# Kernel tuning notes

Measured on AMD Instinct MI355X. Metric: run time of the kernel, lower is better.

Reference implementation:

```python
import jax, jax.numpy as jnp
import numpy as np

C = 10  # cluster gap window; repo-level global constant in the original code


def _per_neuron(v, label):
    """Faithful vectorized translation of the per-(batch,neuron) Python loops.

    v:     [T] membrane potential trace
    label: scalar int target cluster count
    Returns (loss_contribution, num_cluster).
    """
    T = v.shape[0]
    t = jnp.arange(T, dtype=jnp.int32)
    spk = v >= 0.0                                   # spike positions (v >= 0)
    # exclusive prefix counts of spikes: csp[i] = #spikes in v[:i]
    csp = jnp.concatenate([jnp.zeros(1, jnp.int32), jnp.cumsum(spk.astype(jnp.int32))])
    lo = jnp.clip(t - C, 0, T)
    # a spike starts a new cluster iff no spike in the preceding C steps
    cnt_prev = csp[t] - csp[lo]
    is_start = spk & (cnt_prev == 0)
    num_cluster = jnp.sum(is_start.astype(jnp.int32))
    vmax = jnp.max(v)

    # ---- excess branch (label > num_cluster) ----
    # mask[t] = 1 iff some spike lies in [t-C, t+C]  (union of [first-C, last+C] per cluster)
    hi = jnp.clip(t + C + 1, 0, T)
    mask = (csp[hi] - csp[lo]) > 0
    full0 = jnp.all(mask)
    NEG = jnp.asarray(-1e30, v.dtype)
    m0 = jnp.max(jnp.where(mask, NEG, v))            # max over unmasked times (iter 0)
    tm = jnp.argmax(v)                               # original uses global argmax of v
    win = (t >= tm - C // 2) & (t <= tm + C // 2)
    mask2 = mask | win                               # mask after first loop iteration (fixed thereafter)
    full2 = jnp.all(mask2)
    # if mask2 full, remaining iterations pick a spike value (random in original; spikes have v>=0,
    # we use the deterministic surrogate vmax which is always a spike value when spikes exist)
    m_rest = jnp.where(full2, vmax, jnp.max(jnp.where(mask2, NEG, v)))
    label_f = label.astype(v.dtype)
    ncf = num_cluster.astype(v.dtype)
    dE = jnp.maximum(label_f - ncf, 1.0)             # safe denominator (branch-gated below)
    mean_excess = (m0 + (dE - 1.0) * m_rest) / dE
    excess_loss = jnp.where(full0, vmax, -mean_excess)

    # ---- deficit branch (label < num_cluster) ----
    BIG = T + 2 * C + 2
    lt = jax.lax.cummax(jnp.where(spk, t, -BIG))                 # nearest spike <= t
    rt = jax.lax.cummin(jnp.where(spk, t, BIG)[::-1])[::-1]      # nearest spike >= t
    in_span = (rt - lt) <= C                                     # t inside [first,last] of a cluster
    cid = jnp.cumsum(is_start.astype(jnp.int32)) - 1             # cluster id at time t
    K = T // (C + 1) + 1                                         # max possible clusters
    seg = jnp.where(in_span, cid, K)
    rec = jax.ops.segment_max(v, seg, num_segments=K + 1)[:K]    # per-cluster span max
    POS = jnp.asarray(1e30, v.dtype)
    rec = jnp.where(jnp.arange(K) < num_cluster, rec, POS)
    rec = jnp.sort(rec)                                          # ascending, real clusters first
    dD = jnp.maximum(ncf - label_f, 1.0)
    deficit_loss = jnp.sum(jnp.where(jnp.arange(K) < (num_cluster - label), rec, 0.0)) / dD

    contrib = jnp.where(label > num_cluster, excess_loss,
                        jnp.where(label < num_cluster, deficit_loss, 0.0))
    return contrib, num_cluster


def setup_inputs() -> dict:
    key = jax.random.key(0)
    k1, k2, k3 = jax.random.split(key, 3)
    B, T, N = 256, 500, 128
    vmem = jax.random.normal(k1, (B, T, N), dtype=jnp.float32)
    vlastmem = jax.random.normal(k2, (B, T, N), dtype=jnp.float32)
    labels_t = jax.random.randint(k3, (B, N), 0, 5, dtype=jnp.int32)
    return {"vmem": vmem, "vlastmem": vlastmem, "labels_t": labels_t, "ratio": 1}


def reference(vmem, vlastmem, labels_t, ratio):
    # vlastmem and ratio are unused in the original forward; kept for signature fidelity.
    vv = jnp.transpose(vmem, (0, 2, 1))  # [B, N, T]
    contrib, nclus = jax.vmap(jax.vmap(_per_neuron))(vv, labels_t)
    loss = jnp.sum(contrib)
    spike_output = nclus.astype(jnp.float32)  # [B, N] cluster counts
    return loss, spike_output
```

## Files before the change

kernel.cpp:

```cpp
#include <hip/hip_runtime.h>

namespace {
constexpr int CC    = 10;
constexpr int TT    = 500;
constexpr int NN    = 128;
constexpr int G     = 10;
constexpr int LSEG  = TT / G;
constexpr int HALO  = CC;
constexpr int NSLOT = 10;
constexpr int MAXG  = TT / (CC + 1) + 1;
}

__global__ __launch_bounds__(128, 5)
void seg_scan_kernel(const float* __restrict__ vmem, float* __restrict__ ws) {
    const int s   = blockIdx.x;
    const int b   = blockIdx.y;
    const int tid = threadIdx.x;
    const int a   = s * LSEG;
    const float* __restrict__ col = vmem + (size_t)b * TT * NN + tid;

    __shared__ float stg[5 * NN];

    float b0[10], b1[10], b2[10], b3[10] = {};
    auto load = [&](float (&d)[10], int c) {
        #pragma unroll
        for (int j = 0; j < 10; ++j) {
            int t = a + (-HALO + 10 * c + j);
            t = t < 0 ? 0 : (t > TT - 1 ? TT - 1 : t);
            d[j] = col[(size_t)t * NN];
        }
    };

    int   ls = -(1 << 20), lcount = 0, hdne = 0, tmn = 0, hasu = 0;
    float ccm = -1e30f, rmax = -1e30f, hdm = -1e30f, vmx = -1e30f, m0 = -1e30f;
    const bool firstSeg = (s == 0), lastSeg = (s == G - 1);
    #pragma unroll
    for (int i = 0; i < 5; ++i) stg[i * NN + tid] = 0.0f;

    auto scan = [&](const float (&cur)[10], const float (&prev)[10], int c) {
        #pragma unroll
        for (int j = 0; j < 10; ++j) {
            const int ofs = -HALO + 10 * c + j;
            const int t   = a + ofs;
            float v = cur[j];
            if ((ofs < 0 && firstSeg) || (ofs >= LSEG && lastSeg)) v = -1.0f;
            const bool spike = v >= 0.0f;
            if (ofs >= 0 && ofs < LSEG) {
                const float rm2 = fmaxf(rmax, v);
                if (spike) {
                    if (t - ls > CC) {
                        if (lcount > 0) stg[(lcount - 1) * NN + tid] = ccm;
                        ccm = v; ++lcount;
                    } else if (lcount == 0) { hdne = 1; hdm = fmaxf(hdm, rm2); }
                    else ccm = fmaxf(ccm, rm2);
                    rmax = -1e30f;
                } else rmax = rm2;
                if (v > vmx) { vmx = v; tmn = t; }
            }
            if (spike) ls = t;
            if (ofs >= HALO) {
                const float vu = prev[j];
                if (ls < t - 2 * CC) { hasu = 1; if (vu > m0) m0 = vu; }
            }
        }
    };

    load(b0, 0); load(b1, 1);
    load(b2, 2); scan(b0, b3, 0);
    load(b3, 3); scan(b1, b0, 1);
    load(b0, 4); scan(b2, b1, 2);
    load(b1, 5); scan(b3, b2, 3);
    load(b2, 6); scan(b0, b3, 4);
    scan(b1, b0, 5);
    scan(b2, b1, 6);

    if (lcount > 0) stg[(lcount - 1) * NN + tid] = ccm;

    float* __restrict__ wsl = ws + (size_t)(b * G + s) * NSLOT * NN + tid;
    #pragma unroll
    for (int i = 0; i < 5; ++i) wsl[i * NN] = stg[i * NN + tid];
    const int packed = lcount | (hdne << 3) | (hasu << 4) | (tmn << 5);
    wsl[5 * NN] = __int_as_float(packed);
    wsl[6 * NN] = hdm;
    wsl[7 * NN] = rmax;
    wsl[8 * NN] = vmx;
    wsl[9 * NN] = m0;
}

__global__ __launch_bounds__(64)
void merge_kernel(const float* __restrict__ vmem, const float* __restrict__ ws,
                  const int* __restrict__ labels, float* __restrict__ out) {
    const int bb = blockIdx.x, lane = threadIdx.x;
    const int b = bb >> 1, n = ((bb & 1) << 6) | lane;
    __shared__ float gl[MAXG * 64];
    __shared__ float wb[512];

    const float* __restrict__ wsb = ws + (size_t)b * G * NSLOT * NN + n;
    float f[2][10];
    auto loadSeg = [&](int slot, int s2) {
        const float* p = wsb + (size_t)s2 * NSLOT * NN;
        #pragma unroll
        for (int i = 0; i < 10; ++i) f[slot][i] = p[i * NN];
    };
    loadSeg(0, 0);

    int g = 0, g_nc = 0, g_hasu = 0, g_tm = 0;
    bool open = false; float cur = -1e30f, ptg = -1e30f;
    float g_vmax = -1e30f, g_m0 = -1e30f;
    #pragma unroll
    for (int s2 = 0; s2 < G; ++s2) {
        if (s2 + 1 < G) loadSeg((s2 + 1) & 1, s2 + 1);
        const float (&d)[10] = f[s2 & 1];
        const int pk = __float_as_int(d[5]);
        const int k = pk & 7, hne = (pk >> 3) & 1;
        g_nc += k; g_hasu |= (pk >> 4) & 1;
        if (d[8] > g_vmax) { g_vmax = d[8]; g_tm = pk >> 5; }
        if (d[9] > g_m0) g_m0 = d[9];
        if (open) {
            if (hne) { cur = fmaxf(cur, fmaxf(ptg, d[6])); ptg = d[7]; }
            if (k > 0 || !hne) { gl[g * 64 + lane] = cur; ++g; open = false; }
        }
        if (k > 0) {
            #pragma unroll
            for (int i = 0; i < 4; ++i)
                if (i < k - 1) { gl[g * 64 + lane] = d[i]; ++g; }
            float last = d[4];
            if (k == 1) last = d[0];
            else if (k == 2) last = d[1];
            else if (k == 3) last = d[2];
            else if (k == 4) last = d[3];
            cur = last; open = true; ptg = d[7];
        }
    }
    if (open) { gl[g * 64 + lane] = cur; ++g; }

    const int label = labels[b * NN + n];

    const bool need2 = (label > g_nc) && g_hasu && (label - g_nc >= 2);
    float mrest = g_vmax;
    unsigned long long bal = __ballot(need2);
    const float* colbase = vmem + (size_t)b * TT * NN;
    while (bal) {
        const int fl = __ffsll((unsigned long long)bal) - 1;
        bal &= bal - 1;
        const int   nf    = ((bb & 1) << 6) | fl;
        const int   tmf   = __shfl(g_tm, fl);
        const float vmaxf = __shfl(g_vmax, fl);
        #pragma unroll
        for (int j = 0; j < 8; ++j) {
            const int t = lane * 8 + j;
            wb[t] = (t < TT) ? colbase[(size_t)t * NN + nf] : -1.0f;
        }
        __syncthreads();
        int ls2 = -1000, lh = 0; float lm = -1e30f;
        const int u0 = lane * 8;
        for (int t2 = u0 - 10; t2 < u0 + 18; ++t2) {
            const float v = (t2 >= 0 && t2 < 512) ? wb[t2] : -1.0f;
            if (v >= 0.0f) ls2 = t2;
            const int u = t2 - 10;
            if (u >= u0 && u < u0 + 8 && u < TT) {
                if (ls2 < u - 10 && (u < tmf - CC / 2 || u > tmf + CC / 2)) {
                    lh = 1; const float vu = wb[u]; if (vu > lm) lm = vu;
                }
            }
        }
        #pragma unroll
        for (int off = 32; off > 0; off >>= 1) {
            lm = fmaxf(lm, __shfl_down(lm, off));
            lh |= __shfl_down(lh, off);
        }
        const float res = __shfl(lh ? lm : vmaxf, 0);
        if (lane == fl) mrest = res;
        __syncthreads();
    }

    float contrib = 0.0f;
    if (label > g_nc) {
        if (!g_hasu) contrib = g_vmax;
        else {
            const float dE = (float)(label - g_nc);
            contrib = -((g_m0 + (dE - 1.0f) * mrest) / dE);
        }
    } else if (label < g_nc) {
        const int kk = g_nc - label;
        float ssum = 0.0f;
        for (int i = 0; i < kk; ++i) {
            float mn = 1e30f; int mj = 0;
            for (int jj = 0; jj < g_nc; ++jj) {
                const float x = gl[jj * 64 + lane];
                if (x < mn) { mn = x; mj = jj; }
            }
            ssum += mn; gl[mj * 64 + lane] = 1e30f;
        }
        contrib = ssum / (float)kk;
    }

    out[1 + b * NN + n] = (float)g_nc;

    float w = contrib;
    #pragma unroll
    for (int off = 32; off > 0; off >>= 1) w += __shfl_down(w, off);
    if (lane == 0) atomicAdd(out, w);
}

extern "C" void kernel_launch(void* const* d_in, const int* in_sizes, int n_in,
                              void* d_out, int out_size, void* d_ws, size_t ws_size,
                              hipStream_t stream) {
    const float* vmem   = (const float*)d_in[0];
    const int*   labels = (const int*)d_in[2];
    float*       out    = (float*)d_out;
    float*       ws     = (float*)d_ws;

    const int B = in_sizes[2] / NN;

    hipMemsetAsync(out, 0, sizeof(float), stream);
    hipLaunchKernelGGL(seg_scan_kernel, dim3(G, B), dim3(NN), 0, stream, vmem, ws);
    hipLaunchKernelGGL(merge_kernel, dim3(2 * B), dim3(64), 0, stream, vmem, ws, labels, out);
}
```

Baseline: 163.6 us.

## Fuse segment scan and merge into one kernel using shared memory

Replaces the two-kernel pipeline (segment scan writing to a global workspace, then a merge kernel) with a single kernel per batch. Four 128-thread groups each scan a 125-step segment and publish their summaries through shared memory, and one group then performs the merge. This removes the workspace round trip and the second launch, and it adds sched_barrier-controlled load/scan interleaving. The cost is fewer blocks (B=256 with 512 threads each), longer serial scans per thread, and idle threads during the merge.

```diff
diff --git a/kernel.cpp b/kernel.cpp
--- a/kernel.cpp
+++ b/kernel.cpp
@@ -4,38 +4,51 @@
 constexpr int CC    = 10;
 constexpr int TT    = 500;
 constexpr int NN    = 128;
-constexpr int G     = 10;
-constexpr int LSEG  = TT / G;
+constexpr int NG    = 4;
+constexpr int LSEG  = TT / NG;
 constexpr int HALO  = CC;
-constexpr int NSLOT = 10;
+constexpr int NCH   = 15;
+constexpr int MAXK  = 12;
 constexpr int MAXG  = TT / (CC + 1) + 1;
 }
 
-__global__ __launch_bounds__(128, 5)
-void seg_scan_kernel(const float* __restrict__ vmem, float* __restrict__ ws) {
-    const int s   = blockIdx.x;
-    const int b   = blockIdx.y;
+__global__ __launch_bounds__(512, 2)
+void fused_kernel(const float* __restrict__ vmem, const int* __restrict__ labels,
+                  float* __restrict__ out) {
     const int tid = threadIdx.x;
-    const int a   = s * LSEG;
-    const float* __restrict__ col = vmem + (size_t)b * TT * NN + tid;
-
-    __shared__ float stg[5 * NN];
+    const int g   = tid >> 7;
+    const int n   = tid & 127;
+    const int b   = blockIdx.x;
+    const int a   = g * LSEG;
+    const bool firstSeg = (g == 0), lastSeg = (g == NG - 1);
+    const float* __restrict__ col = vmem + (size_t)b * TT * NN + n;
+
+    __shared__ float s_cl[NG][MAXK][NN];
+    __shared__ int   s_pk[NG][NN];
+    __shared__ float s_hdm[NG][NN], s_tg[NG][NN], s_vm[NG][NN], s_m0[NG][NN];
+    __shared__ float s_gl[MAXG][NN];
+    __shared__ float wb[2][512];
+    __shared__ float red[2];
 
     float b0[10], b1[10], b2[10], b3[10] = {};
+
     auto load = [&](float (&d)[10], int c) {
-        #pragma unroll
-        for (int j = 0; j < 10; ++j) {
-            int t = a + (-HALO + 10 * c + j);
-            t = t < 0 ? 0 : (t > TT - 1 ? TT - 1 : t);
-            d[j] = col[(size_t)t * NN];
+        if ((firstSeg && c == 0) || (lastSeg && c >= 13)) {
+            #pragma unroll
+            for (int j = 0; j < 10; ++j) {
+                int t = a - HALO + 10 * c + j;
+                t = t < 0 ? 0 : (t > TT - 1 ? TT - 1 : t);
+                d[j] = col[t * NN];
+            }
+        } else {
+            const float* __restrict__ p = col + (a - HALO + 10 * c) * NN;
+            #pragma unroll
+            for (int j = 0; j < 10; ++j) d[j] = p[j * NN];
         }
     };
 
     int   ls = -(1 << 20), lcount = 0, hdne = 0, tmn = 0, hasu = 0;
     float ccm = -1e30f, rmax = -1e30f, hdm = -1e30f, vmx = -1e30f, m0 = -1e30f;
-    const bool firstSeg = (s == 0), lastSeg = (s == G - 1);
-    #pragma unroll
-    for (int i = 0; i < 5; ++i) stg[i * NN + tid] = 0.0f;
 
     auto scan = [&](const float (&cur)[10], const float (&prev)[10], int c) {
         #pragma unroll
@@ -49,7 +62,7 @@
                 const float rm2 = fmaxf(rmax, v);
                 if (spike) {
                     if (t - ls > CC) {
-                        if (lcount > 0) stg[(lcount - 1) * NN + tid] = ccm;
+                        if (lcount > 0) s_cl[g][lcount - 1][n] = ccm;
                         ccm = v; ++lcount;
                     } else if (lcount == 0) { hdne = 1; hdm = fmaxf(hdm, rm2); }
                     else ccm = fmaxf(ccm, rm2);
@@ -58,149 +71,137 @@
                 if (v > vmx) { vmx = v; tmn = t; }
             }
             if (spike) ls = t;
-            if (ofs >= HALO) {
+            if (ofs >= HALO && ofs < LSEG + HALO) {
                 const float vu = prev[j];
                 if (ls < t - 2 * CC) { hasu = 1; if (vu > m0) m0 = vu; }
             }
         }
     };
 
-    load(b0, 0); load(b1, 1);
-    load(b2, 2); scan(b0, b3, 0);
-    load(b3, 3); scan(b1, b0, 1);
-    load(b0, 4); scan(b2, b1, 2);
-    load(b1, 5); scan(b3, b2, 3);
-    load(b2, 6); scan(b0, b3, 4);
-    scan(b1, b0, 5);
-    scan(b2, b1, 6);
-
-    if (lcount > 0) stg[(lcount - 1) * NN + tid] = ccm;
-
-    float* __restrict__ wsl = ws + (size_t)(b * G + s) * NSLOT * NN + tid;
-    #pragma unroll
-    for (int i = 0; i < 5; ++i) wsl[i * NN] = stg[i * NN + tid];
-    const int packed = lcount | (hdne << 3) | (hasu << 4) | (tmn << 5);
-    wsl[5 * NN] = __int_as_float(packed);
-    wsl[6 * NN] = hdm;
-    wsl[7 * NN] = rmax;
-    wsl[8 * NN] = vmx;
-    wsl[9 * NN] = m0;
-}
-
-__global__ __launch_bounds__(64)
-void merge_kernel(const float* __restrict__ vmem, const float* __restrict__ ws,
-                  const int* __restrict__ labels, float* __restrict__ out) {
-    const int bb = blockIdx.x, lane = threadIdx.x;
-    const int b = bb >> 1, n = ((bb & 1) << 6) | lane;
-    __shared__ float gl[MAXG * 64];
-    __shared__ float wb[512];
-
-    const float* __restrict__ wsb = ws + (size_t)b * G * NSLOT * NN + n;
-    float f[2][10];
-    auto loadSeg = [&](int slot, int s2) {
-        const float* p = wsb + (size_t)s2 * NSLOT * NN;
+    #define SB __builtin_amdgcn_sched_barrier(0)
+    load(b0, 0);  load(b1, 1);  SB;
+    load(b2, 2);  SB; scan(b0, b3, 0);  SB;
+    load(b3, 3);  SB; scan(b1, b0, 1);  SB;
+    load(b0, 4);  SB; scan(b2, b1, 2);  SB;
+    load(b1, 5);  SB; scan(b3, b2, 3);  SB;
+    load(b2, 6);  SB; scan(b0, b3, 4);  SB;
+    load(b3, 7);  SB; scan(b1, b0, 5);  SB;
+    load(b0, 8);  SB; scan(b2, b1, 6);  SB;
+    load(b1, 9);  SB; scan(b3, b2, 7);  SB;
+    load(b2, 10); SB; scan(b0, b3, 8);  SB;
+    load(b3, 11); SB; scan(b1, b0, 9);  SB;
+    load(b0, 12); SB; scan(b2, b1, 10); SB;
+    load(b1, 13); SB; scan(b3, b2, 11); SB;
+    load(b2, 14); SB; scan(b0, b3, 12); SB;
+    scan(b1, b0, 13); scan(b2, b1, 14);
+    #undef SB
+
+    if (lcount > 0) s_cl[g][lcount - 1][n] = ccm;
+
+    s_pk[g][n]  = lcount | (hdne << 4) | (hasu << 5) | (tmn << 6);
+    s_hdm[g][n] = hdm;
+    s_tg[g][n]  = rmax;
+    s_vm[g][n]  = vmx;
+    s_m0[g][n]  = m0;
+    __syncthreads();
+
+    if (tid < NN) {
+        const int lane = tid & 63, wv = tid >> 6;
+        int gi = 0, g_nc = 0, g_hasu = 0, g_tm = 0;
+        bool open = false; float cur = -1e30f, ptg = -1e30f;
+        float g_vmax = -1e30f, g_m0 = -1e30f;
         #pragma unroll
-        for (int i = 0; i < 10; ++i) f[slot][i] = p[i * NN];
-    };
-    loadSeg(0, 0);
-
-    int g = 0, g_nc = 0, g_hasu = 0, g_tm = 0;
-    bool open = false; float cur = -1e30f, ptg = -1e30f;
-    float g_vmax = -1e30f, g_m0 = -1e30f;
-    #pragma unroll
-    for (int s2 = 0; s2 < G; ++s2) {
-        if (s2 + 1 < G) loadSeg((s2 + 1) & 1, s2 + 1);
-        const float (&d)[10] = f[s2 & 1];
-        const int pk = __float_as_int(d[5]);
-        const int k = pk & 7, hne = (pk >> 3) & 1;
-        g_nc += k; g_hasu |= (pk >> 4) & 1;
-        if (d[8] > g_vmax) { g_vmax = d[8]; g_tm = pk >> 5; }
-        if (d[9] > g_m0) g_m0 = d[9];
-        if (open) {
-            if (hne) { cur = fmaxf(cur, fmaxf(ptg, d[6])); ptg = d[7]; }
-            if (k > 0 || !hne) { gl[g * 64 + lane] = cur; ++g; open = false; }
-        }
-        if (k > 0) {
-            #pragma unroll
-            for (int i = 0; i < 4; ++i)
-                if (i < k - 1) { gl[g * 64 + lane] = d[i]; ++g; }
-            float last = d[4];
-            if (k == 1) last = d[0];
-            else if (k == 2) last = d[1];
-            else if (k == 3) last = d[2];
-            else if (k == 4) last = d[3];
-            cur = last; open = true; ptg = d[7];
-        }
+        for (int s = 0; s < NG; ++s) {
+            const int pk = s_pk[s][tid];
+            const int k = pk & 15, hne = (pk >> 4) & 1;
+            g_nc += k; g_hasu |= (pk >> 5) & 1;
+            const float vmS = s_vm[s][tid];
+            if (vmS > g_vmax) { g_vmax = vmS; g_tm = pk >> 6; }
+            const float m0S = s_m0[s][tid];
+            if (m0S > g_m0) g_m0 = m0S;
+            if (open) {
+                if (hne) { cur = fmaxf(cur, fmaxf(ptg, s_hdm[s][tid])); ptg = s_tg[s][tid]; }
+                if (k > 0 || !hne) { s_gl[gi][tid] = cur; ++gi; open = false; }
+            }
+            if (k > 0) {
+                for (int i = 0; i < k - 1; ++i) { s_gl[gi][tid] = s_cl[s][i][tid]; ++gi; }
+                cur = s_cl[s][k - 1][tid]; open = true; ptg = s_tg[s][tid];
+            }
+        }
+        if (open) { s_gl[gi][tid] = cur; ++gi; }
+
+        const int label = labels[b * NN + tid];
+
+        const bool need2 = (label > g_nc) && g_hasu && (label - g_nc >= 2);
+        float mrest = g_vmax;
+        unsigned long long bal = __ballot(need2);
+        const float* colbase = vmem + (size_t)b * TT * NN;
+        float* __restrict__ wbp = wb[wv];
+        while (bal) {
+            const int fl = __ffsll((unsigned long long)bal) - 1;
+            bal &= bal - 1;
+            const int   nf    = (wv << 6) | fl;
+            const int   tmf   = __shfl(g_tm, fl);
+            const float vmaxf = __shfl(g_vmax, fl);
+            #pragma unroll
+            for (int j = 0; j < 8; ++j) {
+                const int t = lane * 8 + j;
+                wbp[t] = (t < TT) ? colbase[(size_t)t * NN + nf] : -1.0f;
+            }
+            asm volatile("s_waitcnt lgkmcnt(0)" ::: "memory");
+            __builtin_amdgcn_wave_barrier();
+            int ls2 = -1000, lh = 0; float lm = -1e30f;
+            const int u0 = lane * 8;
+            for (int t2 = u0 - 10; t2 < u0 + 18; ++t2) {
+                const float v = (t2 >= 0 && t2 < 512) ? wbp[t2] : -1.0f;
+                if (v >= 0.0f) ls2 = t2;
+                const int u = t2 - 10;
+                if (u >= u0 && u < u0 + 8 && u < TT) {
+                    if (ls2 < u - 10 && (u < tmf - CC / 2 || u > tmf + CC / 2)) {
+                        lh = 1; const float vu = wbp[u]; if (vu > lm) lm = vu;
+                    }
+                }
+            }
+            #pragma unroll
+            for (int off = 32; off > 0; off >>= 1) {
+                lm = fmaxf(lm, __shfl_down(lm, off));
+                lh |= __shfl_down(lh, off);
+            }
+            const float res = __shfl(lh ? lm : vmaxf, 0);
+            if (lane == fl) mrest = res;
+            __builtin_amdgcn_wave_barrier();
+        }
+
+        float contrib = 0.0f;
+        if (label > g_nc) {
+            if (!g_hasu) contrib = g_vmax;
+            else {
+                const float dE = (float)(label - g_nc);
+                contrib = -((g_m0 + (dE - 1.0f) * mrest) / dE);
+            }
+        } else if (label < g_nc) {
+            const int kk = g_nc - label;
+            float ssum = 0.0f;
+            for (int i = 0; i < kk; ++i) {
+                float mn = 1e30f; int mj = 0;
+                for (int jj = 0; jj < g_nc; ++jj) {
+                    const float x = s_gl[jj][tid];
+                    if (x < mn) { mn = x; mj = jj; }
+                }
+                ssum += mn; s_gl[mj][tid] = 1e30f;
+            }
+            contrib = ssum / (float)kk;
+        }
+
+        out[1 + b * NN + tid] = (float)g_nc;
+
+        float w = contrib;
+        #pragma unroll
+        for (int off = 32; off > 0; off >>= 1) w += __shfl_down(w, off);
+        if (lane == 0) red[wv] = w;
     }
-    if (open) { gl[g * 64 + lane] = cur; ++g; }
-
-    const int label = labels[b * NN + n];
-
-    const bool need2 = (label > g_nc) && g_hasu && (label - g_nc >= 2);
-    float mrest = g_vmax;
-    unsigned long long bal = __ballot(need2);
-    const float* colbase = vmem + (size_t)b * TT * NN;
-    while (bal) {
-        const int fl = __ffsll((unsigned long long)bal) - 1;
-        bal &= bal - 1;
-        const int   nf    = ((bb & 1) << 6) | fl;
-        const int   tmf   = __shfl(g_tm, fl);
-        const float vmaxf = __shfl(g_vmax, fl);
-        #pragma unroll
-        for (int j = 0; j < 8; ++j) {
-            const int t = lane * 8 + j;
-            wb[t] = (t < TT) ? colbase[(size_t)t * NN + nf] : -1.0f;
-        }
-        __syncthreads();
-        int ls2 = -1000, lh = 0; float lm = -1e30f;
-        const int u0 = lane * 8;
-        for (int t2 = u0 - 10; t2 < u0 + 18; ++t2) {
-            const float v = (t2 >= 0 && t2 < 512) ? wb[t2] : -1.0f;
-            if (v >= 0.0f) ls2 = t2;
-            const int u = t2 - 10;
-            if (u >= u0 && u < u0 + 8 && u < TT) {
-                if (ls2 < u - 10 && (u < tmf - CC / 2 || u > tmf + CC / 2)) {
-                    lh = 1; const float vu = wb[u]; if (vu > lm) lm = vu;
-                }
-            }
-        }
-        #pragma unroll
-        for (int off = 32; off > 0; off >>= 1) {
-            lm = fmaxf(lm, __shfl_down(lm, off));
-            lh |= __shfl_down(lh, off);
-        }
-        const float res = __shfl(lh ? lm : vmaxf, 0);
-        if (lane == fl) mrest = res;
-        __syncthreads();
-    }
-
-    float contrib = 0.0f;
-    if (label > g_nc) {
-        if (!g_hasu) contrib = g_vmax;
-        else {
-            const float dE = (float)(label - g_nc);
-            contrib = -((g_m0 + (dE - 1.0f) * mrest) / dE);
-        }
-    } else if (label < g_nc) {
-        const int kk = g_nc - label;
-        float ssum = 0.0f;
-        for (int i = 0; i < kk; ++i) {
-            float mn = 1e30f; int mj = 0;
-            for (int jj = 0; jj < g_nc; ++jj) {
-                const float x = gl[jj * 64 + lane];
-                if (x < mn) { mn = x; mj = jj; }
-            }
-            ssum += mn; gl[mj * 64 + lane] = 1e30f;
-        }
-        contrib = ssum / (float)kk;
-    }
-
-    out[1 + b * NN + n] = (float)g_nc;
-
-    float w = contrib;
-    #pragma unroll
-    for (int off = 32; off > 0; off >>= 1) w += __shfl_down(w, off);
-    if (lane == 0) atomicAdd(out, w);
+    __syncthreads();
+    if (tid == 0) atomicAdd(out, red[0] + red[1]);
 }
 
 extern "C" void kernel_launch(void* const* d_in, const int* in_sizes, int n_in,
@@ -209,11 +210,10 @@
     const float* vmem   = (const float*)d_in[0];
     const int*   labels = (const int*)d_in[2];
     float*       out    = (float*)d_out;
-    float*       ws     = (float*)d_ws;
+    (void)d_ws; (void)ws_size;
 
     const int B = in_sizes[2] / NN;
 
     hipMemsetAsync(out, 0, sizeof(float), stream);
-    hipLaunchKernelGGL(seg_scan_kernel, dim3(G, B), dim3(NN), 0, stream, vmem, ws);
-    hipLaunchKernelGGL(merge_kernel, dim3(2 * B), dim3(64), 0, stream, vmem, ws, labels, out);
+    hipLaunchKernelGGL(fused_kernel, dim3(B), dim3(512), 0, stream, vmem, labels, out);
 }
```

After: 160.4 us (median of 2 runs). About the same (-1.9%).

## Vectorize segment scan to float4 per thread and batch merge loads

Applied to the files above, without the earlier changes.

The segment-scan kernel now has each thread process four neurons with float4 loads, two batches per 64-thread block. This cuts the number of load instructions and improves memory-transaction width, but quadruples per-thread register state and drops occupancy hints. The merge kernel now issues all 100 workspace loads up front and hoists the label load ahead of the merge loop. It also replaces block-level __syncthreads with wave barriers plus an explicit lgkmcnt wait, which is valid because the block is a single wave. Sched barriers pin the load/compute interleave.

```diff
diff --git a/kernel.cpp b/kernel.cpp
--- a/kernel.cpp
+++ b/kernel.cpp
@@ -11,83 +11,122 @@
 constexpr int MAXG  = TT / (CC + 1) + 1;
 }
 
-__global__ __launch_bounds__(128, 5)
-void seg_scan_kernel(const float* __restrict__ vmem, float* __restrict__ ws) {
-    const int s   = blockIdx.x;
-    const int b   = blockIdx.y;
-    const int tid = threadIdx.x;
-    const int a   = s * LSEG;
-    const float* __restrict__ col = vmem + (size_t)b * TT * NN + tid;
-
-    __shared__ float stg[5 * NN];
-
-    float b0[10], b1[10], b2[10], b3[10] = {};
-    auto load = [&](float (&d)[10], int c) {
-        #pragma unroll
-        for (int j = 0; j < 10; ++j) {
-            int t = a + (-HALO + 10 * c + j);
-            t = t < 0 ? 0 : (t > TT - 1 ? TT - 1 : t);
-            d[j] = col[(size_t)t * NN];
+static __device__ __forceinline__ float comp(const float4& v, int k) {
+    return k == 0 ? v.x : k == 1 ? v.y : k == 2 ? v.z : v.w;
+}
+
+__global__ __launch_bounds__(64, 2)
+void seg_scan4(const float* __restrict__ vmem, float* __restrict__ ws) {
+    const int s  = blockIdx.x;
+    const int bp = blockIdx.y;
+    const int l  = threadIdx.x;
+    const int b  = bp * 2 + (l >> 5);
+    const int n4 = l & 31;
+    const int a  = s * LSEG;
+    const bool firstSeg = (s == 0), lastSeg = (s == G - 1);
+    const float4* __restrict__ col4 = (const float4*)vmem + (size_t)b * TT * 32 + n4;
+
+    __shared__ float stg[5][64][4];
+    #pragma unroll
+    for (int i = 0; i < 5; ++i)
+        #pragma unroll
+        for (int k = 0; k < 4; ++k) stg[i][l][k] = 0.0f;
+
+    float4 b0[10], b1[10], b2[10], b3[10] = {};
+
+    auto load = [&](float4 (&d)[10], int c) {
+        if ((firstSeg && c == 0) || (lastSeg && c == 6)) {
+            #pragma unroll
+            for (int j = 0; j < 10; ++j) {
+                int t = a + (-HALO + 10 * c + j);
+                t = t < 0 ? 0 : (t > TT - 1 ? TT - 1 : t);
+                d[j] = col4[t * 32];
+            }
+        } else {
+            const float4* __restrict__ p = col4 + (a - HALO + 10 * c) * 32;
+            #pragma unroll
+            for (int j = 0; j < 10; ++j) d[j] = p[j * 32];
         }
     };
 
-    int   ls = -(1 << 20), lcount = 0, hdne = 0, tmn = 0, hasu = 0;
-    float ccm = -1e30f, rmax = -1e30f, hdm = -1e30f, vmx = -1e30f, m0 = -1e30f;
-    const bool firstSeg = (s == 0), lastSeg = (s == G - 1);
-    #pragma unroll
-    for (int i = 0; i < 5; ++i) stg[i * NN + tid] = 0.0f;
-
-    auto scan = [&](const float (&cur)[10], const float (&prev)[10], int c) {
+    int   ls[4], lcount[4], hdne[4], tmn[4], hasu[4];
+    float ccm[4], rmax[4], hdm[4], vmx[4], m0[4];
+    #pragma unroll
+    for (int k = 0; k < 4; ++k) {
+        ls[k] = -(1 << 20); lcount[k] = 0; hdne[k] = 0; tmn[k] = 0; hasu[k] = 0;
+        ccm[k] = -1e30f; rmax[k] = -1e30f; hdm[k] = -1e30f; vmx[k] = -1e30f; m0[k] = -1e30f;
+    }
+
+    auto scan = [&](const float4 (&cur)[10], const float4 (&prev)[10], int c) {
         #pragma unroll
         for (int j = 0; j < 10; ++j) {
             const int ofs = -HALO + 10 * c + j;
             const int t   = a + ofs;
-            float v = cur[j];
-            if ((ofs < 0 && firstSeg) || (ofs >= LSEG && lastSeg)) v = -1.0f;
-            const bool spike = v >= 0.0f;
-            if (ofs >= 0 && ofs < LSEG) {
-                const float rm2 = fmaxf(rmax, v);
-                if (spike) {
-                    if (t - ls > CC) {
-                        if (lcount > 0) stg[(lcount - 1) * NN + tid] = ccm;
-                        ccm = v; ++lcount;
-                    } else if (lcount == 0) { hdne = 1; hdm = fmaxf(hdm, rm2); }
-                    else ccm = fmaxf(ccm, rm2);
-                    rmax = -1e30f;
-                } else rmax = rm2;
-                if (v > vmx) { vmx = v; tmn = t; }
-            }
-            if (spike) ls = t;
-            if (ofs >= HALO) {
-                const float vu = prev[j];
-                if (ls < t - 2 * CC) { hasu = 1; if (vu > m0) m0 = vu; }
+            #pragma unroll
+            for (int k = 0; k < 4; ++k) {
+                float v = comp(cur[j], k);
+                if ((ofs < 0 && firstSeg) || (ofs >= LSEG && lastSeg)) v = -1.0f;
+                const bool spike = v >= 0.0f;
+                if (ofs >= 0 && ofs < LSEG) {
+                    const float rm2 = fmaxf(rmax[k], v);
+                    if (spike) {
+                        if (t - ls[k] > CC) {
+                            if (lcount[k] > 0) stg[lcount[k] - 1][l][k] = ccm[k];
+                            ccm[k] = v; ++lcount[k];
+                        } else if (lcount[k] == 0) { hdne[k] = 1; hdm[k] = fmaxf(hdm[k], rm2); }
+                        else ccm[k] = fmaxf(ccm[k], rm2);
+                        rmax[k] = -1e30f;
+                    } else rmax[k] = rm2;
+                    if (v > vmx[k]) { vmx[k] = v; tmn[k] = t; }
+                }
+                if (spike) ls[k] = t;
+                if (ofs >= HALO) {
+                    const float vu = comp(prev[j], k);
+                    if (ls[k] < t - 2 * CC) { hasu[k] = 1; if (vu > m0[k]) m0[k] = vu; }
+                }
             }
         }
     };
 
-    load(b0, 0); load(b1, 1);
-    load(b2, 2); scan(b0, b3, 0);
-    load(b3, 3); scan(b1, b0, 1);
-    load(b0, 4); scan(b2, b1, 2);
-    load(b1, 5); scan(b3, b2, 3);
-    load(b2, 6); scan(b0, b3, 4);
-    scan(b1, b0, 5);
-    scan(b2, b1, 6);
-
-    if (lcount > 0) stg[(lcount - 1) * NN + tid] = ccm;
-
-    float* __restrict__ wsl = ws + (size_t)(b * G + s) * NSLOT * NN + tid;
-    #pragma unroll
-    for (int i = 0; i < 5; ++i) wsl[i * NN] = stg[i * NN + tid];
-    const int packed = lcount | (hdne << 3) | (hasu << 4) | (tmn << 5);
-    wsl[5 * NN] = __int_as_float(packed);
-    wsl[6 * NN] = hdm;
-    wsl[7 * NN] = rmax;
-    wsl[8 * NN] = vmx;
-    wsl[9 * NN] = m0;
-}
-
-__global__ __launch_bounds__(64)
+    #define SB __builtin_amdgcn_sched_barrier(0)
+    load(b0, 0); load(b1, 1); SB;
+    load(b2, 2); SB; scan(b0, b3, 0); SB;
+    load(b3, 3); SB; scan(b1, b0, 1); SB;
+    load(b0, 4); SB; scan(b2, b1, 2); SB;
+    load(b1, 5); SB; scan(b3, b2, 3); SB;
+    load(b2, 6); SB; scan(b0, b3, 4); SB;
+    scan(b1, b0, 5); scan(b2, b1, 6);
+    #undef SB
+
+    #pragma unroll
+    for (int k = 0; k < 4; ++k)
+        if (lcount[k] > 0) stg[lcount[k] - 1][l][k] = ccm[k];
+
+    float* __restrict__ wsl = ws + (size_t)(b * G + s) * NSLOT * NN + n4 * 4;
+    #pragma unroll
+    for (int i = 0; i < 5; ++i) {
+        float4 o;
+        o.x = stg[i][l][0]; o.y = stg[i][l][1]; o.z = stg[i][l][2]; o.w = stg[i][l][3];
+        *(float4*)(wsl + i * NN) = o;
+    }
+    float4 opk, ohdm, otg, ovm, om0;
+    #pragma unroll
+    for (int k = 0; k < 4; ++k) {
+        const float pk = __int_as_float(lcount[k] | (hdne[k] << 3) | (hasu[k] << 4) |
+                                        (tmn[k] << 5));
+        if (k == 0) { opk.x = pk; ohdm.x = hdm[0]; otg.x = rmax[0]; ovm.x = vmx[0]; om0.x = m0[0]; }
+        if (k == 1) { opk.y = pk; ohdm.y = hdm[1]; otg.y = rmax[1]; ovm.y = vmx[1]; om0.y = m0[1]; }
+        if (k == 2) { opk.z = pk; ohdm.z = hdm[2]; otg.z = rmax[2]; ovm.z = vmx[2]; om0.z = m0[2]; }
+        if (k == 3) { opk.w = pk; ohdm.w = hdm[3]; otg.w = rmax[3]; ovm.w = vmx[3]; om0.w = m0[3]; }
+    }
+    *(float4*)(wsl + 5 * NN) = opk;
+    *(float4*)(wsl + 6 * NN) = ohdm;
+    *(float4*)(wsl + 7 * NN) = otg;
+    *(float4*)(wsl + 8 * NN) = ovm;
+    *(float4*)(wsl + 9 * NN) = om0;
+}
+
+__global__ __launch_bounds__(64, 2)
 void merge_kernel(const float* __restrict__ vmem, const float* __restrict__ ws,
                   const int* __restrict__ labels, float* __restrict__ out) {
     const int bb = blockIdx.x, lane = threadIdx.x;
@@ -96,21 +135,19 @@
     __shared__ float wb[512];
 
     const float* __restrict__ wsb = ws + (size_t)b * G * NSLOT * NN + n;
-    float f[2][10];
-    auto loadSeg = [&](int slot, int s2) {
-        const float* p = wsb + (size_t)s2 * NSLOT * NN;
-        #pragma unroll
-        for (int i = 0; i < 10; ++i) f[slot][i] = p[i * NN];
-    };
-    loadSeg(0, 0);
+    float f[G * NSLOT];
+    #pragma unroll
+    for (int q = 0; q < G * NSLOT; ++q) f[q] = wsb[(size_t)q * NN];
+    __builtin_amdgcn_sched_barrier(0);
+
+    const int label = labels[b * NN + n];
 
     int g = 0, g_nc = 0, g_hasu = 0, g_tm = 0;
     bool open = false; float cur = -1e30f, ptg = -1e30f;
     float g_vmax = -1e30f, g_m0 = -1e30f;
     #pragma unroll
     for (int s2 = 0; s2 < G; ++s2) {
-        if (s2 + 1 < G) loadSeg((s2 + 1) & 1, s2 + 1);
-        const float (&d)[10] = f[s2 & 1];
+        const float* d = &f[s2 * NSLOT];
         const int pk = __float_as_int(d[5]);
         const int k = pk & 7, hne = (pk >> 3) & 1;
         g_nc += k; g_hasu |= (pk >> 4) & 1;
@@ -134,14 +171,12 @@
     }
     if (open) { gl[g * 64 + lane] = cur; ++g; }
 
-    const int label = labels[b * NN + n];
-
     const bool need2 = (label > g_nc) && g_hasu && (label - g_nc >= 2);
     float mrest = g_vmax;
     unsigned long long bal = __ballot(need2);
     const float* colbase = vmem + (size_t)b * TT * NN;
     while (bal) {
-        const int fl = __ffsll((unsigned long long)bal) - 1;
+        const int fl = __ffsll(bal) - 1;
         bal &= bal - 1;
         const int   nf    = ((bb & 1) << 6) | fl;
         const int   tmf   = __shfl(g_tm, fl);
@@ -151,7 +186,8 @@
             const int t = lane * 8 + j;
             wb[t] = (t < TT) ? colbase[(size_t)t * NN + nf] : -1.0f;
         }
-        __syncthreads();
+        asm volatile("s_waitcnt lgkmcnt(0)" ::: "memory");
+        __builtin_amdgcn_wave_barrier();
         int ls2 = -1000, lh = 0; float lm = -1e30f;
         const int u0 = lane * 8;
         for (int t2 = u0 - 10; t2 < u0 + 18; ++t2) {
@@ -171,7 +207,7 @@
         }
         const float res = __shfl(lh ? lm : vmaxf, 0);
         if (lane == fl) mrest = res;
-        __syncthreads();
+        __builtin_amdgcn_wave_barrier();
     }
 
     float contrib = 0.0f;
@@ -214,6 +250,7 @@
     const int B = in_sizes[2] / NN;
 
     hipMemsetAsync(out, 0, sizeof(float), stream);
-    hipLaunchKernelGGL(seg_scan_kernel, dim3(G, B), dim3(NN), 0, stream, vmem, ws);
-    hipLaunchKernelGGL(merge_kernel, dim3(2 * B), dim3(64), 0, stream, vmem, ws, labels, out);
-}
+    hipLaunchKernelGGL(seg_scan4, dim3(G, B / 2), dim3(64), 0, stream, vmem, ws);
+    hipLaunchKernelGGL(merge_kernel, dim3(2 * B), dim3(64), 0, stream,
+                       vmem, ws, labels, out);
+}
```

New measurement: 196.7 us. +20.2%, slower.
